# Kernel tuning notes

Hardware: AMD Instinct MI355X
Metric: run time of the kernel (lower is better)

## Reference

```python
import jax, jax.numpy as jnp
import numpy as np

B, N, DIM, HID = 2, 256, 128, 128
EPS = 1e-5

def layer_norm(x, g, b):
    m = jnp.mean(x, axis=-1, keepdims=True)
    v = jnp.mean(jnp.square(x - m), axis=-1, keepdims=True)
    return (x - m) * jax.lax.rsqrt(v + EPS) * g + b

def setup_inputs() -> dict:
    key = jax.random.key(0)
    ks = jax.random.split(key, 8)
    s = 0.02
    return {
        "x": jax.random.normal(ks[0], (B, N, N, DIM), dtype=jnp.float32),
        "src_mask": jnp.ones((B, N), dtype=jnp.int32),
        "ln1_g": jnp.ones((DIM,), jnp.float32),
        "ln1_b": jnp.zeros((DIM,), jnp.float32),
        "Wl": jax.random.normal(ks[1], (DIM, HID), jnp.float32) * s,
        "bl": jnp.zeros((HID,), jnp.float32),
        "Wr": jax.random.normal(ks[2], (DIM, HID), jnp.float32) * s,
        "br": jnp.zeros((HID,), jnp.float32),
        "Wlg": jax.random.normal(ks[3], (DIM, HID), jnp.float32) * s,
        "blg": jnp.ones((HID,), jnp.float32),
        "Wrg": jax.random.normal(ks[4], (DIM, HID), jnp.float32) * s,
        "brg": jnp.ones((HID,), jnp.float32),
        "Wog": jax.random.normal(ks[5], (DIM, HID), jnp.float32) * s,
        "bog": jnp.ones((HID,), jnp.float32),
        "ln2_g": jnp.ones((HID,), jnp.float32),
        "ln2_b": jnp.zeros((HID,), jnp.float32),
        "Wo": jax.random.normal(ks[6], (HID, DIM), jnp.float32) * s,
        "bo": jnp.zeros((DIM,), jnp.float32),
    }

def reference(x, src_mask, ln1_g, ln1_b, Wl, bl, Wr, br, Wlg, blg, Wrg, brg,
              Wog, bog, ln2_g, ln2_b, Wo, bo):
    m = src_mask.astype(jnp.float32)
    # pair mask [B,N,N,1] = outer product of token masks
    mask = (m[:, :, None] * m[:, None, :])[..., None]
    xn = layer_norm(x, ln1_g, ln1_b)                      # [B,N,N,D]
    left = (xn @ Wl + bl) * mask                           # [B,N,N,H]
    right = (xn @ Wr + br) * mask
    left = left * jax.nn.sigmoid(xn @ Wlg + blg)
    right = right * jax.nn.sigmoid(xn @ Wrg + brg)
    out_gate = jax.nn.sigmoid(xn @ Wog + bog)
    # ingoing mix: out[b,i,j,d] = sum_k left[b,k,j,d] * right[b,k,i,d]
    out = jnp.einsum('bkjd,bkid->bijd', left, right)
    out = layer_norm(out, ln2_g, ln2_b) * out_gate
    return out @ Wo + bo
```

## Files before the change

kernel.cpp:

```cpp
#include <hip/hip_runtime.h>
#include <stdint.h>

#define Bn 2
#define Nn 256
#define Dn 128

typedef __attribute__((ext_vector_type(8))) short short8;
typedef __attribute__((ext_vector_type(4))) float f32x4;

__device__ __forceinline__ float sigm(float x){
    return __builtin_amdgcn_rcpf(1.0f + __builtin_amdgcn_exp2f(-1.44269504f*x));
}
__device__ __forceinline__ unsigned short f2b(float f){
    unsigned u = __float_as_uint(f);
    return (unsigned short)((u + 0x7FFFu + ((u>>16)&1u)) >> 16);
}
__device__ __forceinline__ float b2f(unsigned short h){
    return __uint_as_float(((unsigned)h)<<16);
}

__global__ __launch_bounds__(256) void k0_wt(
    const float* __restrict__ Wl, const float* __restrict__ Wr,
    const float* __restrict__ Wlg, const float* __restrict__ Wrg,
    const float* __restrict__ Wog, const float* __restrict__ Wo,
    unsigned short* __restrict__ WTf)
{
    int mat = blockIdx.x >> 3, nt = blockIdx.x & 7;
    const float* W = (mat==0)?Wl:(mat==1)?Wr:(mat==2)?Wlg:(mat==3)?Wrg:(mat==4)?Wog:Wo;
    int t = threadIdx.x;
    int kc = t >> 6, l = t & 63;
    int n  = nt*16 + (l & 15);
    int k0 = kc*32 + (l >> 4)*8;
    short8 sv;
    #pragma unroll
    for (int e=0;e<8;++e) sv[e] = (short)f2b(W[(k0+e)*128 + n]);
    *(short8*)&WTf[(((mat*8 + nt)*4 + kc) << 9) + l*8] = sv;
}

__global__ __launch_bounds__(512, 6) void k1_proj(
    const float* __restrict__ x, const int* __restrict__ msk,
    const float* __restrict__ g1, const float* __restrict__ b1,
    const unsigned short* __restrict__ WTf,
    const float* __restrict__ bl, const float* __restrict__ br,
    const float* __restrict__ blg, const float* __restrict__ brg,
    const float* __restrict__ bog,
    unsigned short* __restrict__ leftT, unsigned short* __restrict__ rightT,
    unsigned short* __restrict__ og)
{
    __shared__ __align__(16) unsigned short xn_s[32][136];
    __shared__ __align__(16) unsigned short lds_l[128][40];
    __shared__ __align__(16) unsigned short lds_r[128][40];
    __shared__ float mask_s[32];

    const int tid = threadIdx.x;
    const int wv = tid>>6, lane = tid&63;
    int bid = blockIdx.x;
    int pb  = bid & 7;
    int q   = (bid >> 3) & 255;
    int b   = bid >> 11;
    int p0  = pb * 32;

    {
        float a0[4], a1[4];
        #pragma unroll
        for (int rr=0; rr<4; ++rr){
            int r = wv*4 + rr;
            long row = ((long)(b*Nn + p0 + r))*Nn + q;
            const float* xr = x + row*Dn;
            a0[rr] = xr[lane]; a1[rr] = xr[lane+64];
        }
        if (lane < 4){
            int r = wv*4 + lane;
            mask_s[r] = (float)(msk[b*Nn + p0 + r] * msk[b*Nn + q]);
        }
        #pragma unroll
        for (int rr=0; rr<4; ++rr){
            int r = wv*4 + rr;
            float s = a0[rr]+a1[rr], sq = a0[rr]*a0[rr] + a1[rr]*a1[rr];
            #pragma unroll
            for (int m=1; m<64; m<<=1){ s += __shfl_xor(s,m); sq += __shfl_xor(sq,m); }
            float mean = s*(1.f/128.f);
            float var  = sq*(1.f/128.f) - mean*mean;
            float rstd = rsqrtf(var + 1e-5f);
            xn_s[r][lane]    = f2b((a0[rr]-mean)*rstd*g1[lane]    + b1[lane]);
            xn_s[r][lane+64] = f2b((a1[rr]-mean)*rstd*g1[lane+64] + b1[lane+64]);
        }
    }
    __syncthreads();

    const int l15 = lane & 15, g = lane >> 4;
    const int n = wv*16 + l15;

    short8 aF[2][4];
    #pragma unroll
    for (int rt=0; rt<2; ++rt)
        #pragma unroll
        for (int kc=0; kc<4; ++kc)
            aF[rt][kc] = *(const short8*)&xn_s[rt*16 + l15][kc*32 + g*8];
    __syncthreads();

    {
        f32x4 aV[2] = {{0.f,0.f,0.f,0.f},{0.f,0.f,0.f,0.f}};
        f32x4 aG[2] = {{0.f,0.f,0.f,0.f},{0.f,0.f,0.f,0.f}};
        #pragma unroll
        for (int kc=0; kc<4; ++kc){
            short8 bF = *(const short8*)&WTf[(((0*8 + wv)*4 + kc) << 9) + lane*8];
            aV[0] = __builtin_amdgcn_mfma_f32_16x16x32_bf16(aF[0][kc], bF, aV[0], 0,0,0);
            aV[1] = __builtin_amdgcn_mfma_f32_16x16x32_bf16(aF[1][kc], bF, aV[1], 0,0,0);
        }
        #pragma unroll
        for (int kc=0; kc<4; ++kc){
            short8 bF = *(const short8*)&WTf[(((2*8 + wv)*4 + kc) << 9) + lane*8];
            aG[0] = __builtin_amdgcn_mfma_f32_16x16x32_bf16(aF[0][kc], bF, aG[0], 0,0,0);
            aG[1] = __builtin_amdgcn_mfma_f32_16x16x32_bf16(aF[1][kc], bF, aG[1], 0,0,0);
        }
        float bv = bl[n], bgv = blg[n];
        #pragma unroll
        for (int rt=0; rt<2; ++rt){
            unsigned short pk[4];
            #pragma unroll
            for (int r=0; r<4; ++r){
                float mk = mask_s[rt*16 + g*4 + r];
                pk[r] = f2b((aV[rt][r] + bv)*mk * sigm(aG[rt][r] + bgv));
            }
            *(ushort4*)&lds_l[n][rt*16 + g*4] = make_ushort4(pk[0],pk[1],pk[2],pk[3]);
        }
    }
    {
        f32x4 aV[2] = {{0.f,0.f,0.f,0.f},{0.f,0.f,0.f,0.f}};
        f32x4 aG[2] = {{0.f,0.f,0.f,0.f},{0.f,0.f,0.f,0.f}};
        #pragma unroll
        for (int kc=0; kc<4; ++kc){
            short8 bF = *(const short8*)&WTf[(((1*8 + wv)*4 + kc) << 9) + lane*8];
            aV[0] = __builtin_amdgcn_mfma_f32_16x16x32_bf16(aF[0][kc], bF, aV[0], 0,0,0);
            aV[1] = __builtin_amdgcn_mfma_f32_16x16x32_bf16(aF[1][kc], bF, aV[1], 0,0,0);
        }
        #pragma unroll
        for (int kc=0; kc<4; ++kc){
            short8 bF = *(const short8*)&WTf[(((3*8 + wv)*4 + kc) << 9) + lane*8];
            aG[0] = __builtin_amdgcn_mfma_f32_16x16x32_bf16(aF[0][kc], bF, aG[0], 0,0,0);
            aG[1] = __builtin_amdgcn_mfma_f32_16x16x32_bf16(aF[1][kc], bF, aG[1], 0,0,0);
        }
        float bv = br[n], bgv = brg[n];
        #pragma unroll
        for (int rt=0; rt<2; ++rt){
            unsigned short pk[4];
            #pragma unroll
            for (int r=0; r<4; ++r){
                float mk = mask_s[rt*16 + g*4 + r];
                pk[r] = f2b((aV[rt][r] + bv)*mk * sigm(aG[rt][r] + bgv));
            }
            *(ushort4*)&lds_r[n][rt*16 + g*4] = make_ushort4(pk[0],pk[1],pk[2],pk[3]);
        }
    }
    {
        f32x4 aV[2] = {{0.f,0.f,0.f,0.f},{0.f,0.f,0.f,0.f}};
        #pragma unroll
        for (int kc=0; kc<4; ++kc){
            short8 bF = *(const short8*)&WTf[(((4*8 + wv)*4 + kc) << 9) + lane*8];
            aV[0] = __builtin_amdgcn_mfma_f32_16x16x32_bf16(aF[0][kc], bF, aV[0], 0,0,0);
            aV[1] = __builtin_amdgcn_mfma_f32_16x16x32_bf16(aF[1][kc], bF, aV[1], 0,0,0);
        }
        float bgv = bog[n];
        #pragma unroll
        for (int rt=0; rt<2; ++rt)
            #pragma unroll
            for (int r=0; r<4; ++r)
                xn_s[rt*16 + g*4 + r][n] = f2b(sigm(aV[rt][r] + bgv));
    }
    __syncthreads();

    {
        int nn = tid >> 2, quad = tid & 3;
        long gbase = (((long)(b*Nn + q))*Dn + nn)*Nn + p0 + quad*8;
        *(short8*)&leftT [gbase] = *(const short8*)&lds_l[nn][quad*8];
        *(short8*)&rightT[gbase] = *(const short8*)&lds_r[nn][quad*8];
    }
    {
        int row = tid >> 4, seg = tid & 15;
        long grow = ((long)(b*Nn + p0 + row))*Nn + q;
        *(short8*)&og[grow*256 + seg*8] = *(const short8*)&xn_s[row][seg*8];
    }
}

__global__ __launch_bounds__(512, 2) void k2_tri(
    const unsigned short* __restrict__ leftT, const unsigned short* __restrict__ rightT,
    unsigned short* __restrict__ tri)
{
    __shared__ __align__(16) char smem[65536];
    unsigned short (*l_s)[64][32] = (unsigned short(*)[64][32])smem;
    unsigned short (*r_s)[64][32] = (unsigned short(*)[64][32])(smem + 32768);

    const int tid = threadIdx.x;
    const int wv = tid>>6, lane = tid&63;
    int f = blockIdx.x;
    int L = (f & 7)*64 + (f >> 3);
    int z = L >> 4, rem = L & 15;
    const int j0 = (rem & 3) * 64, i0 = (rem >> 2) * 64;
    const int db = z & 15, b = z >> 4;
    const int d  = db*8 + wv;
    const int l15 = lane&15, g = lane>>4;

    long rbaseL[4], rbaseR[4];
    int choff[4];
    #pragma unroll
    for (int jj=0; jj<4; ++jj){
        int slot = jj*64 + lane;
        int row = slot >> 2, ch = slot & 3;
        rbaseL[jj] = ((long)((b*Nn + j0 + row)*Dn + d)) << 8;
        rbaseR[jj] = ((long)((b*Nn + i0 + row)*Dn + d)) << 8;
        choff[jj] = ch*8;
    }
    short8* dl = (short8*)&l_s[wv][0][0];
    short8* dr = (short8*)&r_s[wv][0][0];

    f32x4 acc[4][4];
    #pragma unroll
    for (int a=0;a<4;++a)
        #pragma unroll
        for (int c=0;c<4;++c) acc[a][c] = (f32x4){0.f,0.f,0.f,0.f};

    for (int k0 = 0; k0 < Nn; k0 += 32){
        short8 stg[8];
        #pragma unroll
        for (int jj=0; jj<4; ++jj){
            stg[jj]   = *(const short8*)&leftT [rbaseL[jj] + k0 + choff[jj]];
            stg[4+jj] = *(const short8*)&rightT[rbaseR[jj] + k0 + choff[jj]];
        }
        #pragma unroll
        for (int jj=0; jj<4; ++jj){
            int slot = jj*64 + lane;
            dl[slot] = stg[jj];
            dr[slot] = stg[4+jj];
        }
        short8 aF[4];
        #pragma unroll
        for (int jt=0;jt<4;++jt) aF[jt] = *(const short8*)&l_s[wv][jt*16 + l15][g*8];
        #pragma unroll
        for (int it2=0;it2<4;++it2){
            short8 bF = *(const short8*)&r_s[wv][it2*16 + l15][g*8];
            #pragma unroll
            for (int jt=0;jt<4;++jt)
                acc[jt][it2] = __builtin_amdgcn_mfma_f32_16x16x32_bf16(aF[jt], bF, acc[jt][it2], 0,0,0);
        }
    }
    __syncthreads();

    unsigned short* tsb = (unsigned short*)smem;
    #pragma unroll
    for (int jt=0;jt<4;++jt){
        #pragma unroll
        for (int it2=0;it2<4;++it2){
            int iloc = it2*16 + l15;
            int rowid = iloc*8 + wv;
            int slotw = (2*jt + (g>>1)) ^ (iloc & 7);
            ushort4 v = make_ushort4(f2b(acc[jt][it2][0]), f2b(acc[jt][it2][1]),
                                     f2b(acc[jt][it2][2]), f2b(acc[jt][it2][3]));
            *(ushort4*)&tsb[rowid*64 + slotw*8 + (g&1)*4] = v;
        }
    }
    __syncthreads();

    long gb = ((((long)(b*16+db))*Nn + i0)*8)*Nn + j0;
    #pragma unroll
    for (int itr=0; itr<8; ++itr){
        int rowid = itr*64 + (tid>>3);
        int jseg  = tid & 7;
        int i_loc = rowid >> 3;
        short8 val = *(const short8*)&tsb[rowid*64 + ((jseg ^ (i_loc&7))*8)];
        *(short8*)&tri[gb + (long)rowid*Nn + jseg*8] = val;
    }
}

__global__ __launch_bounds__(256, 3) void k3_out(
    const unsigned short* __restrict__ tri, const unsigned short* __restrict__ ogu,
    const float* __restrict__ g2, const float* __restrict__ b2,
    const unsigned short* __restrict__ WTf, const float* __restrict__ bo,
    float* __restrict__ out)
{
    __shared__ __align__(16) unsigned short trn_s[32][136];
    __shared__ __align__(16) unsigned short xn_s[32][160];
    __shared__ __align__(16) float out_s[32][132];

    const int tid = threadIdx.x;
    int bid = blockIdx.x;
    int jb = bid & 7, i = (bid>>3) & 255, b = bid >> 11;
    int j0 = jb*32;

    {
        int dfull = tid >> 1, jh = tid & 1;
        int db = dfull >> 3, dd = dfull & 7;
        long base = ((((long)(b*16+db))*Nn + i)*8 + dd)*Nn + j0 + jh*16;
        union { short8 s8[2]; unsigned short u[16]; } v;
        v.s8[0] = *(const short8*)&tri[base];
        v.s8[1] = *(const short8*)&tri[base+8];
        #pragma unroll
        for (int jj=0;jj<16;++jj) trn_s[jh*16+jj][dfull] = v.u[jj];
    }
    __syncthreads();

    const int wv = tid>>6, lane = tid&63;
    #pragma unroll
    for (int rr=0; rr<8; ++rr){
        int r = wv*8 + rr;
        float v0 = b2f(trn_s[r][lane]), v1 = b2f(trn_s[r][lane+64]);
        float s = v0+v1, sq = v0*v0+v1*v1;
        #pragma unroll
        for (int m=1; m<64; m<<=1){ s += __shfl_xor(s,m); sq += __shfl_xor(sq,m); }
        float mean = s*(1.f/128.f);
        float var  = sq*(1.f/128.f) - mean*mean;
        float rstd = rsqrtf(var + 1e-5f);
        long grow = ((long)(b*Nn + i))*Nn + j0 + r;
        float o0 = b2f(ogu[grow*256 + lane]);
        float o1 = b2f(ogu[grow*256 + lane + 64]);
        xn_s[r][lane]    = f2b(((v0-mean)*rstd*g2[lane]    + b2[lane])   *o0);
        xn_s[r][lane+64] = f2b(((v1-mean)*rstd*g2[lane+64] + b2[lane+64])*o1);
    }
    __syncthreads();

    const int l15 = lane&15, g = lane>>4;
    const int it = wv>>1, nh = wv&1;
    short8 aF[4];
    #pragma unroll
    for (int kc=0; kc<4; ++kc)
        aF[kc] = *(const short8*)&xn_s[it*16 + l15][kc*32 + g*8];
    #pragma unroll
    for (int nt=0; nt<4; ++nt){
        int n0 = nh*64 + nt*16;
        f32x4 c = {0.f,0.f,0.f,0.f};
        #pragma unroll
        for (int kc=0; kc<4; ++kc){
            short8 bF = *(const short8*)&WTf[(((40 + nh*4 + nt)*4 + kc) << 9) + lane*8];
            c = __builtin_amdgcn_mfma_f32_16x16x32_bf16(aF[kc], bF, c, 0,0,0);
        }
        float bov = bo[n0 + l15];
        #pragma unroll
        for (int r=0;r<4;++r)
            out_s[it*16 + g*4 + r][n0 + l15] = c[r] + bov;
    }
    __syncthreads();

    {
        int row = tid>>3, seg = tid&7;
        long grow = ((long)(b*Nn + i))*Nn + j0 + row;
        #pragma unroll
        for (int e=0;e<4;++e){
            f32x4 v = *(f32x4*)&out_s[row][seg*16 + e*4];
            *(f32x4*)&out[grow*Dn + seg*16 + e*4] = v;
        }
    }
}

extern "C" void kernel_launch(void* const* d_in, const int* in_sizes, int n_in,
                              void* d_out, int out_size, void* d_ws, size_t ws_size,
                              hipStream_t stream)
{
    const float* x   = (const float*)d_in[0];
    const int*   msk = (const int*)  d_in[1];
    const float* g1  = (const float*)d_in[2];
    const float* b1  = (const float*)d_in[3];
    const float* Wl  = (const float*)d_in[4];
    const float* bl  = (const float*)d_in[5];
    const float* Wr  = (const float*)d_in[6];
    const float* br  = (const float*)d_in[7];
    const float* Wlg = (const float*)d_in[8];
    const float* blg = (const float*)d_in[9];
    const float* Wrg = (const float*)d_in[10];
    const float* brg = (const float*)d_in[11];
    const float* Wog = (const float*)d_in[12];
    const float* bog = (const float*)d_in[13];
    const float* g2  = (const float*)d_in[14];
    const float* b2  = (const float*)d_in[15];
    const float* Wo  = (const float*)d_in[16];
    const float* bo  = (const float*)d_in[17];

    float* out = (float*)d_out;
    unsigned short* ogu = (unsigned short*)d_out;
    char* wsb = (char*)d_ws;
    unsigned short* leftT  = (unsigned short*)wsb;
    unsigned short* rightT = (unsigned short*)(wsb + 33554432);
    unsigned short* tri    = (unsigned short*)(wsb + 67108864);
    unsigned short* WTf    = (unsigned short*)(wsb + 100663296);

    hipLaunchKernelGGL(k0_wt, dim3(48), dim3(256), 0, stream,
                       Wl, Wr, Wlg, Wrg, Wog, Wo, WTf);
    hipLaunchKernelGGL(k1_proj, dim3(Bn*Nn*8), dim3(512), 0, stream,
                       x, msk, g1, b1, WTf, bl, br, blg, brg, bog,
                       leftT, rightT, ogu);
    hipLaunchKernelGGL(k2_tri, dim3(512), dim3(512), 0, stream,
                       leftT, rightT, tri);
    hipLaunchKernelGGL(k3_out, dim3(Bn*Nn*8), dim3(256), 0, stream,
                       tri, ogu, g2, b2, WTf, bo, out);
}
```

Measured before the change: 130.4 us.

## Double k1 projection tile to 64 rows per block and use intrinsic bf16 conversion

The projection kernel now processes 64 p-rows per block instead of 32, halving the grid and doubling the MFMA row tiles per wave. Each weight fragment loaded from global is reused across four row tiles instead of two, and stores to leftT/rightT/og move 32-byte contiguous chunks. The bf16 rounding helper switches to the HIP intrinsic conversion. In exchange there is more register and LDS pressure, a lower occupancy hint, and fewer blocks to hide latency.

```diff
diff --git a/kernel.cpp b/kernel.cpp
--- a/kernel.cpp
+++ b/kernel.cpp
@@ -1,4 +1,5 @@
 #include <hip/hip_runtime.h>
+#include <hip/hip_bf16.h>
 #include <stdint.h>
 
 #define Bn 2
@@ -12,8 +13,8 @@
     return __builtin_amdgcn_rcpf(1.0f + __builtin_amdgcn_exp2f(-1.44269504f*x));
 }
 __device__ __forceinline__ unsigned short f2b(float f){
-    unsigned u = __float_as_uint(f);
-    return (unsigned short)((u + 0x7FFFu + ((u>>16)&1u)) >> 16);
+    __hip_bfloat16 h = __float2bfloat16(f);
+    return __builtin_bit_cast(unsigned short, h);
 }
 __device__ __forceinline__ float b2f(unsigned short h){
     return __uint_as_float(((unsigned)h)<<16);
@@ -37,7 +38,7 @@
     *(short8*)&WTf[(((mat*8 + nt)*4 + kc) << 9) + l*8] = sv;
 }
 
-__global__ __launch_bounds__(512, 6) void k1_proj(
+__global__ __launch_bounds__(512, 4) void k1_proj(
     const float* __restrict__ x, const int* __restrict__ msk,
     const float* __restrict__ g1, const float* __restrict__ b1,
     const unsigned short* __restrict__ WTf,
@@ -47,35 +48,35 @@
     unsigned short* __restrict__ leftT, unsigned short* __restrict__ rightT,
     unsigned short* __restrict__ og)
 {
-    __shared__ __align__(16) unsigned short xn_s[32][136];
-    __shared__ __align__(16) unsigned short lds_l[128][40];
-    __shared__ __align__(16) unsigned short lds_r[128][40];
-    __shared__ float mask_s[32];
+    __shared__ __align__(16) unsigned short xn_s[64][136];
+    __shared__ __align__(16) unsigned short lds_l[128][72];
+    __shared__ __align__(16) unsigned short lds_r[128][72];
+    __shared__ float mask_s[64];
 
     const int tid = threadIdx.x;
     const int wv = tid>>6, lane = tid&63;
     int bid = blockIdx.x;
-    int pb  = bid & 7;
-    int q   = (bid >> 3) & 255;
-    int b   = bid >> 11;
-    int p0  = pb * 32;
-
-    {
-        float a0[4], a1[4];
-        #pragma unroll
-        for (int rr=0; rr<4; ++rr){
-            int r = wv*4 + rr;
+    int pb  = bid & 3;
+    int q   = (bid >> 2) & 255;
+    int b   = bid >> 10;
+    int p0  = pb * 64;
+
+    {
+        float a0[8], a1[8];
+        #pragma unroll
+        for (int rr=0; rr<8; ++rr){
+            int r = wv*8 + rr;
             long row = ((long)(b*Nn + p0 + r))*Nn + q;
             const float* xr = x + row*Dn;
             a0[rr] = xr[lane]; a1[rr] = xr[lane+64];
         }
-        if (lane < 4){
-            int r = wv*4 + lane;
+        if (lane < 8){
+            int r = wv*8 + lane;
             mask_s[r] = (float)(msk[b*Nn + p0 + r] * msk[b*Nn + q]);
         }
         #pragma unroll
-        for (int rr=0; rr<4; ++rr){
-            int r = wv*4 + rr;
+        for (int rr=0; rr<8; ++rr){
+            int r = wv*8 + rr;
             float s = a0[rr]+a1[rr], sq = a0[rr]*a0[rr] + a1[rr]*a1[rr];
             #pragma unroll
             for (int m=1; m<64; m<<=1){ s += __shfl_xor(s,m); sq += __shfl_xor(sq,m); }
@@ -91,32 +92,34 @@
     const int l15 = lane & 15, g = lane >> 4;
     const int n = wv*16 + l15;
 
-    short8 aF[2][4];
-    #pragma unroll
-    for (int rt=0; rt<2; ++rt)
+    short8 aF[4][4];
+    #pragma unroll
+    for (int rt=0; rt<4; ++rt)
         #pragma unroll
         for (int kc=0; kc<4; ++kc)
             aF[rt][kc] = *(const short8*)&xn_s[rt*16 + l15][kc*32 + g*8];
     __syncthreads();
 
     {
-        f32x4 aV[2] = {{0.f,0.f,0.f,0.f},{0.f,0.f,0.f,0.f}};
-        f32x4 aG[2] = {{0.f,0.f,0.f,0.f},{0.f,0.f,0.f,0.f}};
+        f32x4 aV[4] = {{0,0,0,0},{0,0,0,0},{0,0,0,0},{0,0,0,0}};
+        f32x4 aG[4] = {{0,0,0,0},{0,0,0,0},{0,0,0,0},{0,0,0,0}};
         #pragma unroll
         for (int kc=0; kc<4; ++kc){
             short8 bF = *(const short8*)&WTf[(((0*8 + wv)*4 + kc) << 9) + lane*8];
-            aV[0] = __builtin_amdgcn_mfma_f32_16x16x32_bf16(aF[0][kc], bF, aV[0], 0,0,0);
-            aV[1] = __builtin_amdgcn_mfma_f32_16x16x32_bf16(aF[1][kc], bF, aV[1], 0,0,0);
+            #pragma unroll
+            for (int rt=0; rt<4; ++rt)
+                aV[rt] = __builtin_amdgcn_mfma_f32_16x16x32_bf16(aF[rt][kc], bF, aV[rt], 0,0,0);
         }
         #pragma unroll
         for (int kc=0; kc<4; ++kc){
             short8 bF = *(const short8*)&WTf[(((2*8 + wv)*4 + kc) << 9) + lane*8];
-            aG[0] = __builtin_amdgcn_mfma_f32_16x16x32_bf16(aF[0][kc], bF, aG[0], 0,0,0);
-            aG[1] = __builtin_amdgcn_mfma_f32_16x16x32_bf16(aF[1][kc], bF, aG[1], 0,0,0);
+            #pragma unroll
+            for (int rt=0; rt<4; ++rt)
+                aG[rt] = __builtin_amdgcn_mfma_f32_16x16x32_bf16(aF[rt][kc], bF, aG[rt], 0,0,0);
         }
         float bv = bl[n], bgv = blg[n];
         #pragma unroll
-        for (int rt=0; rt<2; ++rt){
+        for (int rt=0; rt<4; ++rt){
             unsigned short pk[4];
             #pragma unroll
             for (int r=0; r<4; ++r){
@@ -127,23 +130,25 @@
         }
     }
     {
-        f32x4 aV[2] = {{0.f,0.f,0.f,0.f},{0.f,0.f,0.f,0.f}};
-        f32x4 aG[2] = {{0.f,0.f,0.f,0.f},{0.f,0.f,0.f,0.f}};
+        f32x4 aV[4] = {{0,0,0,0},{0,0,0,0},{0,0,0,0},{0,0,0,0}};
+        f32x4 aG[4] = {{0,0,0,0},{0,0,0,0},{0,0,0,0},{0,0,0,0}};
         #pragma unroll
         for (int kc=0; kc<4; ++kc){
             short8 bF = *(const short8*)&WTf[(((1*8 + wv)*4 + kc) << 9) + lane*8];
-            aV[0] = __builtin_amdgcn_mfma_f32_16x16x32_bf16(aF[0][kc], bF, aV[0], 0,0,0);
-            aV[1] = __builtin_amdgcn_mfma_f32_16x16x32_bf16(aF[1][kc], bF, aV[1], 0,0,0);
+            #pragma unroll
+            for (int rt=0; rt<4; ++rt)
+                aV[rt] = __builtin_amdgcn_mfma_f32_16x16x32_bf16(aF[rt][kc], bF, aV[rt], 0,0,0);
         }
         #pragma unroll
         for (int kc=0; kc<4; ++kc){
             short8 bF = *(const short8*)&WTf[(((3*8 + wv)*4 + kc) << 9) + lane*8];
-            aG[0] = __builtin_amdgcn_mfma_f32_16x16x32_bf16(aF[0][kc], bF, aG[0], 0,0,0);
-            aG[1] = __builtin_amdgcn_mfma_f32_16x16x32_bf16(aF[1][kc], bF, aG[1], 0,0,0);
+            #pragma unroll
+            for (int rt=0; rt<4; ++rt)
+                aG[rt] = __builtin_amdgcn_mfma_f32_16x16x32_bf16(aF[rt][kc], bF, aG[rt], 0,0,0);
         }
         float bv = br[n], bgv = brg[n];
         #pragma unroll
-        for (int rt=0; rt<2; ++rt){
+        for (int rt=0; rt<4; ++rt){
             unsigned short pk[4];
             #pragma unroll
             for (int r=0; r<4; ++r){
@@ -154,16 +159,17 @@
         }
     }
     {
-        f32x4 aV[2] = {{0.f,0.f,0.f,0.f},{0.f,0.f,0.f,0.f}};
+        f32x4 aV[4] = {{0,0,0,0},{0,0,0,0},{0,0,0,0},{0,0,0,0}};
         #pragma unroll
         for (int kc=0; kc<4; ++kc){
             short8 bF = *(const short8*)&WTf[(((4*8 + wv)*4 + kc) << 9) + lane*8];
-            aV[0] = __builtin_amdgcn_mfma_f32_16x16x32_bf16(aF[0][kc], bF, aV[0], 0,0,0);
-            aV[1] = __builtin_amdgcn_mfma_f32_16x16x32_bf16(aF[1][kc], bF, aV[1], 0,0,0);
+            #pragma unroll
+            for (int rt=0; rt<4; ++rt)
+                aV[rt] = __builtin_amdgcn_mfma_f32_16x16x32_bf16(aF[rt][kc], bF, aV[rt], 0,0,0);
         }
         float bgv = bog[n];
         #pragma unroll
-        for (int rt=0; rt<2; ++rt)
+        for (int rt=0; rt<4; ++rt)
             #pragma unroll
             for (int r=0; r<4; ++r)
                 xn_s[rt*16 + g*4 + r][n] = f2b(sigm(aV[rt][r] + bgv));
@@ -172,14 +178,17 @@
 
     {
         int nn = tid >> 2, quad = tid & 3;
-        long gbase = (((long)(b*Nn + q))*Dn + nn)*Nn + p0 + quad*8;
-        *(short8*)&leftT [gbase] = *(const short8*)&lds_l[nn][quad*8];
-        *(short8*)&rightT[gbase] = *(const short8*)&lds_r[nn][quad*8];
-    }
-    {
-        int row = tid >> 4, seg = tid & 15;
+        long gbase = (((long)(b*Nn + q))*Dn + nn)*Nn + p0 + quad*16;
+        *(short8*)&leftT [gbase]     = *(const short8*)&lds_l[nn][quad*16];
+        *(short8*)&leftT [gbase + 8] = *(const short8*)&lds_l[nn][quad*16 + 8];
+        *(short8*)&rightT[gbase]     = *(const short8*)&lds_r[nn][quad*16];
+        *(short8*)&rightT[gbase + 8] = *(const short8*)&lds_r[nn][quad*16 + 8];
+    }
+    {
+        int row = tid >> 3, seg = tid & 7;
         long grow = ((long)(b*Nn + p0 + row))*Nn + q;
-        *(short8*)&og[grow*256 + seg*8] = *(const short8*)&xn_s[row][seg*8];
+        *(short8*)&og[grow*256 + seg*16]     = *(const short8*)&xn_s[row][seg*16];
+        *(short8*)&og[grow*256 + seg*16 + 8] = *(const short8*)&xn_s[row][seg*16 + 8];
     }
 }
 
@@ -384,7 +393,7 @@
 
     hipLaunchKernelGGL(k0_wt, dim3(48), dim3(256), 0, stream,
                        Wl, Wr, Wlg, Wrg, Wog, Wo, WTf);
-    hipLaunchKernelGGL(k1_proj, dim3(Bn*Nn*8), dim3(512), 0, stream,
+    hipLaunchKernelGGL(k1_proj, dim3(Bn*Nn*4), dim3(512), 0, stream,
                        x, msk, g1, b1, WTf, bl, br, blg, brg, bog,
                        leftT, rightT, ogu);
     hipLaunchKernelGGL(k2_tri, dim3(512), dim3(512), 0, stream,
```

Result: slower. 135.3 us (+3.7%).
